# Kernel optimization log

Measured on AMD Instinct MI355X. Metric: run time of the kernel, lower is better.

The kernel has to match this reference:

```python
import jax, jax.numpy as jnp
import numpy as np

NUM_EMBEDDINGS = 8192
EMBEDDING_DIM = 64
COMMITMENT_COST = 0.25


def setup_inputs() -> dict:
    key = jax.random.key(0)
    k1, k2 = jax.random.split(key)
    hidden_states = jax.random.normal(k1, (32, 32, 32, EMBEDDING_DIM), dtype=jnp.float32)
    init_bound = 1.0 / NUM_EMBEDDINGS
    embedding = jax.random.uniform(k2, (NUM_EMBEDDINGS, EMBEDDING_DIM), dtype=jnp.float32,
                                   minval=-init_bound, maxval=init_bound)
    return {"hidden_states": hidden_states, "embedding": embedding}


def reference(hidden_states, embedding):
    # hidden_states: (B, H, W, D); embedding: (K, D)
    flat = hidden_states.reshape(-1, EMBEDDING_DIM)            # (N, D)
    z_sq = jnp.sum(flat * flat, axis=1, keepdims=True)          # (N, 1)
    e_sq = jnp.sum(embedding * embedding, axis=1)               # (K,)
    # squared L2 distances: ||z||^2 + ||e||^2 - 2 z.e
    distances = z_sq + e_sq - 2.0 * (flat @ embedding.T)        # (N, K)
    encoding_indices = jnp.argmin(distances, axis=1)            # (N,)
    # one-hot @ embedding == gather; identical math, efficient form
    quantized = jnp.take(embedding, encoding_indices, axis=0).reshape(hidden_states.shape)
    # codebook + commitment loss (return_loss=True path)
    loss = (jnp.mean((jax.lax.stop_gradient(quantized) - hidden_states) ** 2)
            + COMMITMENT_COST * jnp.mean((quantized - jax.lax.stop_gradient(hidden_states)) ** 2))
    # straight-through estimator
    z_q = hidden_states + jax.lax.stop_gradient(quantized - hidden_states)
    B = hidden_states.shape[0]
    min_encoding_indices = encoding_indices.reshape(B, -1)      # (B, num_tokens)
    return z_q, min_encoding_indices, loss
```

## Files before the change

kernel.cpp:

```cpp
#include <hip/hip_runtime.h>
#include <cfloat>

#define N_TOK   32768
#define DIM     64
#define K_CODES 8192
#define NCHK    64
#define TPB     128

#define IDX_OFF  (N_TOK * DIM)
#define LOSS_OFF (N_TOK * DIM + N_TOK)

#define WS_ESQ   0
#define WS_EHIT  8192
#define WS_PART  270336

#define MRG   2e-5f
#define DINIT 6e-5f

typedef __attribute__((ext_vector_type(8)))  short bf16x8;
typedef __attribute__((ext_vector_type(16))) float f32x16;

__device__ inline ushort f2bf(float x) {
    unsigned u = __float_as_uint(x);
    return (ushort)((u + 0x7FFFu + ((u >> 16) & 1u)) >> 16);
}
__device__ inline float bf2f(ushort h) { return __uint_as_float(((unsigned)h) << 16); }
__device__ inline ushort f2bf_up(float x) {
    unsigned u = __float_as_uint(x);
    return (x >= 0.0f) ? (ushort)((u + 0xFFFFu) >> 16) : (ushort)(u >> 16);
}
__device__ inline unsigned long long packdi(float d, int i) {
    unsigned u = __float_as_uint(d);
    u ^= (u & 0x80000000u) ? 0xFFFFFFFFu : 0x80000000u;
    return ((unsigned long long)u << 32) | (unsigned)i;
}

__global__ __launch_bounds__(256) void esq_kernel(const float* __restrict__ emb,
                                                  float* __restrict__ esq) {
#pragma clang fp contract(off)
    const int tid = threadIdx.x;
    const int q = tid & 7;
    const int code = blockIdx.x * 32 + (tid >> 3);
    const float* row = emb + code * DIM;
    float x = row[q];
    float r = x * x;
#pragma unroll
    for (int m = 1; m < 8; ++m) {
        float y = row[q + 8 * m];
        float sq = y * y;
        r = r + sq;
    }
    r = r + __shfl_xor(r, 1, 64);
    r = r + __shfl_xor(r, 2, 64);
    r = r + __shfl_xor(r, 4, 64);
    if (q == 0) esq[code] = r;
}

__global__ __launch_bounds__(256) void pack2(const float* __restrict__ emb,
                                             ushort* __restrict__ ehiT,
                                             float* __restrict__ eT) {
#pragma clang fp contract(off)
    const int k = blockIdx.x * 256 + threadIdx.x;
    float v[64];
    {
        const float4* ep = (const float4*)(emb + (size_t)k * DIM);
#pragma unroll
        for (int i = 0; i < 16; ++i) {
            const float4 a = ep[i];
            v[4 * i] = a.x; v[4 * i + 1] = a.y; v[4 * i + 2] = a.z; v[4 * i + 3] = a.w;
        }
    }
#pragma unroll
    for (int j = 0; j < 64; ++j) eT[(size_t)j * K_CODES + k] = v[j];
    const int sc = k >> 7, lc = k & 127;
#pragma unroll
    for (int q = 0; q < 4; ++q)
#pragma unroll
        for (int h = 0; h < 2; ++h) {
            bf16x8 o;
#pragma unroll
            for (int e = 0; e < 8; ++e) o[e] = (short)f2bf(v[16 * q + 8 * h + e]);
            *(bf16x8*)(ehiT + ((((size_t)sc * 4 + q) * 2 + h) * 128 + lc) * 8) = o;
        }
}

__global__ __launch_bounds__(256, 2) void vq_mfma(const float* __restrict__ hid,
                                                  const ushort* __restrict__ ehiT,
                                                  ushort* __restrict__ Mm) {
#pragma clang fp contract(off)
    const int tid = threadIdx.x;
    const int lane = tid & 63;
    const int w = tid >> 6;
    const int h = lane >> 5;
    const int t0 = blockIdx.x * 64;

    bf16x8 z_hi[2][4], z_lo[2][4];
#pragma unroll
    for (int ts = 0; ts < 2; ++ts)
#pragma unroll
    for (int q = 0; q < 4; ++q) {
        const float* zp = hid + (size_t)(t0 + 32 * ts + (lane & 31)) * DIM + 16 * q + 8 * h;
        const float4 u0 = *(const float4*)zp;
        const float4 u1 = *(const float4*)(zp + 4);
        const float zz[8] = {u0.x, u0.y, u0.z, u0.w, u1.x, u1.y, u1.z, u1.w};
        bf16x8 hv, lv;
#pragma unroll
        for (int i = 0; i < 8; ++i) {
            const ushort hb = f2bf(zz[i]);
            hv[i] = (short)hb;
            lv[i] = (short)f2bf(zz[i] - bf2f(hb));
        }
        z_hi[ts][q] = hv; z_lo[ts][q] = lv;
    }

    f32x16 zc;
#pragma unroll
    for (int i = 0; i < 16; ++i) zc[i] = 0.0f;

    for (int g = 0; g < 16; ++g) {
        const int sc = 4 * g + w;
        float wm0 = -3.0e38f, wm1 = -3.0e38f;
#pragma unroll
        for (int r = 0; r < 4; ++r) {
            bf16x8 A[4];
#pragma unroll
            for (int q = 0; q < 4; ++q)
                A[q] = *(const bf16x8*)(ehiT +
                        ((((size_t)sc * 4 + q) * 2 + h) * 128 + 32 * r + (lane & 31)) * 8);
            f32x16 d0, d1;
#pragma unroll
            for (int q = 0; q < 4; ++q) {
                if (q == 0) {
                    d0 = __builtin_amdgcn_mfma_f32_32x32x16_bf16(A[0], z_hi[0][0], zc, 0, 0, 0);
                    d1 = __builtin_amdgcn_mfma_f32_32x32x16_bf16(A[0], z_hi[1][0], zc, 0, 0, 0);
                } else {
                    d0 = __builtin_amdgcn_mfma_f32_32x32x16_bf16(A[q], z_hi[0][q], d0, 0, 0, 0);
                    d1 = __builtin_amdgcn_mfma_f32_32x32x16_bf16(A[q], z_hi[1][q], d1, 0, 0, 0);
                }
                d0 = __builtin_amdgcn_mfma_f32_32x32x16_bf16(A[q], z_lo[0][q], d0, 0, 0, 0);
                d1 = __builtin_amdgcn_mfma_f32_32x32x16_bf16(A[q], z_lo[1][q], d1, 0, 0, 0);
            }
#pragma unroll
            for (int i = 0; i < 16; ++i) {
                wm0 = fmaxf(wm0, d0[i]);
                wm1 = fmaxf(wm1, d1[i]);
            }
        }
        wm0 = fmaxf(wm0, __shfl_xor(wm0, 32, 64));
        wm1 = fmaxf(wm1, __shfl_xor(wm1, 32, 64));
        if (lane < 32) {
            Mm[(size_t)sc * N_TOK + t0 + lane]      = f2bf_up(wm0);
            Mm[(size_t)sc * N_TOK + t0 + 32 + lane] = f2bf_up(wm1);
        }
    }
}

__global__ __launch_bounds__(512, 1) void vq_select(const float* __restrict__ hid,
                                                    const float* __restrict__ eT,
                                                    const float* __restrict__ esq,
                                                    const ushort* __restrict__ Mm,
                                                    float* __restrict__ out_idx) {
#pragma clang fp contract(off)
    __shared__ float z_s[TPB][68];
    __shared__ float zsq_s[TPB];
    __shared__ float eps_s[TPB];
    __shared__ float bD_s[TPB];
    __shared__ float mxw[4][TPB];
    __shared__ unsigned long long key_s[TPB];
    __shared__ unsigned long long m0_s[NCHK];
    __shared__ unsigned long long m1_s[NCHK];

    const int tid = threadIdx.x;
    const int lane = tid & 63;
    const int w = tid >> 6;
    const int t0 = blockIdx.x * TPB;

    {
        const int t = tid >> 2;
        const int j4 = (tid & 3) * 4;
        const float4* src = (const float4*)(hid + (size_t)(t0 + t) * DIM);
        float4* dst = (float4*)(&z_s[t][0]);
#pragma unroll
        for (int i = 0; i < 4; ++i) dst[j4 + i] = src[j4 + i];
    }
    if (tid < TPB) key_s[tid] = ~0ull;
    __syncthreads();

    {
        const int token = tid & 127;
        const int cg = tid >> 7;
        float pm = bf2f(Mm[(size_t)(16 * cg) * N_TOK + t0 + token]);
#pragma unroll 5
        for (int c = 16 * cg + 1; c < 16 * cg + 16; ++c)
            pm = fmaxf(pm, bf2f(Mm[(size_t)c * N_TOK + t0 + token]));
        mxw[cg][token] = pm;
    }
    if (tid < TPB) {
        const float* zr = &z_s[tid][0];
        float r[8];
#pragma unroll
        for (int q = 0; q < 8; ++q) {
            float x = zr[q]; r[q] = x * x;
#pragma unroll
            for (int m = 1; m < 8; ++m) {
                float y = zr[q + 8 * m];
                float sq = y * y;
                r[q] = r[q] + sq;
            }
        }
        zsq_s[tid] = ((r[0] + r[1]) + (r[2] + r[3])) + ((r[4] + r[5]) + (r[6] + r[7]));
    }
    __syncthreads();
    if (tid < TPB) {
        const float mx = fmaxf(fmaxf(mxw[0][tid], mxw[1][tid]),
                               fmaxf(mxw[2][tid], mxw[3][tid]));
        const float zsq = zsq_s[tid];
        const float eps = sqrtf(zsq) * 2.5e-6f + 2e-7f;
        eps_s[tid] = eps;
        bD_s[tid] = zsq - 2.0f * mx + 2.0f * eps + DINIT;
    }
    __syncthreads();

#pragma unroll
    for (int i = 0; i < 8; ++i) {
        const int c = 8 * w + i;
        const float mA = bf2f(Mm[(size_t)c * N_TOK + t0 + lane]);
        const int sA = (fmaf(-2.0f, mA + eps_s[lane], zsq_s[lane]) - MRG) < bD_s[lane];
        const unsigned long long b0 = __ballot(sA);
        const float mB = bf2f(Mm[(size_t)c * N_TOK + t0 + 64 + lane]);
        const int sB = (fmaf(-2.0f, mB + eps_s[64 + lane], zsq_s[64 + lane]) - MRG) < bD_s[64 + lane];
        const unsigned long long b1 = __ballot(sB);
        if (lane == 0) { m0_s[c] = b0; m1_s[c] = b1; }
    }

    for (int i = 0; i < 8; ++i) {
        const int c = 8 * w + i;
        unsigned long long msk0 = m0_s[c], msk1 = m1_s[c];
        if (!(msk0 | msk1)) continue;
        const int k0 = c * 128 + 2 * lane;
        const float* eb = eT + k0;
        const float2 es2 = *(const float2*)(esq + k0);

        while (msk0 | msk1) {
            int G = 1;
            int tA, tB;
            if (msk0) { tA = __ffsll(msk0) - 1; msk0 &= msk0 - 1; }
            else      { tA = 64 + __ffsll(msk1) - 1; msk1 &= msk1 - 1; }
            tB = tA;
            if (msk0 | msk1) {
                G = 2;
                if (msk0) { tB = __ffsll(msk0) - 1; msk0 &= msk0 - 1; }
                else      { tB = 64 + __ffsll(msk1) - 1; msk1 &= msk1 - 1; }
            }
            const float4* zpA = (const float4*)(&z_s[tA][0]);
            const float4* zpB = (const float4*)(&z_s[tB][0]);

            float2 bA[8], bB[8];
            float aA0, aA1, aB0, aB1;
#define LOADG(B, G2) { _Pragma("unroll") \
    for (int j = 0; j < 8; ++j) \
        B[j] = *(const float2*)(eb + (size_t)(8 * (G2) + j) * K_CODES); }
#define FMAJ(Bj, vA, vB, COMP) \
    aA0 = fmaf(vA.COMP, Bj.x, aA0); aA1 = fmaf(vA.COMP, Bj.y, aA1); \
    aB0 = fmaf(vB.COMP, Bj.x, aB0); aB1 = fmaf(vB.COMP, Bj.y, aB1);
#define FMAG(B, G2) { \
    const float4 vA = zpA[2 * (G2)], vB = zpB[2 * (G2)]; \
    FMAJ(B[0], vA, vB, x) FMAJ(B[1], vA, vB, y) \
    FMAJ(B[2], vA, vB, z) FMAJ(B[3], vA, vB, w) \
    const float4 uA = zpA[2 * (G2) + 1], uB = zpB[2 * (G2) + 1]; \
    FMAJ(B[4], uA, uB, x) FMAJ(B[5], uA, uB, y) \
    FMAJ(B[6], uA, uB, z) FMAJ(B[7], uA, uB, w) }

            LOADG(bA, 0)
            LOADG(bB, 1)
            {
                const float4 vA = zpA[0], vB = zpB[0];
                aA0 = vA.x * bA[0].x; aA1 = vA.x * bA[0].y;
                aB0 = vB.x * bA[0].x; aB1 = vB.x * bA[0].y;
                FMAJ(bA[1], vA, vB, y)
                FMAJ(bA[2], vA, vB, z)
                FMAJ(bA[3], vA, vB, w)
                const float4 uA = zpA[1], uB = zpB[1];
                FMAJ(bA[4], uA, uB, x)
                FMAJ(bA[5], uA, uB, y)
                FMAJ(bA[6], uA, uB, z)
                FMAJ(bA[7], uA, uB, w)
            }
            LOADG(bA, 2) FMAG(bB, 1)
            LOADG(bB, 3) FMAG(bA, 2)
            LOADG(bA, 4) FMAG(bB, 3)
            LOADG(bB, 5) FMAG(bA, 4)
            LOADG(bA, 6) FMAG(bB, 5)
            LOADG(bB, 7) FMAG(bA, 6)
            FMAG(bB, 7)
#undef LOADG
#undef FMAJ
#undef FMAG

#define FINISH(aX0, aX1, tX) { \
    const float zqX = zsq_s[tX]; \
    const float dX0 = fmaf(-2.0f, aX0, zqX + es2.x); \
    const float dX1 = fmaf(-2.0f, aX1, zqX + es2.y); \
    float dl = dX0; int il = k0; \
    if (dX1 < dl) { dl = dX1; il = k0 + 1; } \
    _Pragma("unroll") \
    for (int mm = 1; mm < 64; mm <<= 1) { \
        const float ov = __shfl_xor(dl, mm, 64); \
        const int   oi = __shfl_xor(il, mm, 64); \
        if (ov < dl || (ov == dl && oi < il)) { dl = ov; il = oi; } \
    } \
    if (lane == 0) atomicMin(&key_s[tX], packdi(dl, il)); }

            FINISH(aA0, aA1, tA)
            if (G > 1) FINISH(aB0, aB1, tB)
#undef FINISH
        }
    }
    __syncthreads();

    if (tid < TPB) out_idx[t0 + tid] = (float)(int)(key_s[tid] & 0xFFFFFFFFull);
}

__global__ __launch_bounds__(256) void vq_finish(const float* __restrict__ hid,
                                                 const float* __restrict__ emb,
                                                 const float* __restrict__ out_idx,
                                                 float* __restrict__ out_zq,
                                                 float* __restrict__ partials) {
#pragma clang fp contract(off)
    __shared__ float lred[4];
    const int tid = threadIdx.x;
    const int t = blockIdx.x * 256 + tid;

    const int bi = (int)out_idx[t];

    const float4* q4 = (const float4*)(emb + (size_t)bi * DIM);
    const float4* h4 = (const float4*)(hid + (size_t)t * DIM);
    float4* o4 = (float4*)(out_zq + (size_t)t * DIM);
    float lsum = 0.f;
#pragma unroll
    for (int i = 0; i < 16; ++i) {
        const float4 q = q4[i];
        const float4 h = h4[i];
        float4 zq;
        float dx;
        dx = q.x - h.x; zq.x = h.x + dx; lsum += dx * dx;
        dx = q.y - h.y; zq.y = h.y + dx; lsum += dx * dx;
        dx = q.z - h.z; zq.z = h.z + dx; lsum += dx * dx;
        dx = q.w - h.w; zq.w = h.w + dx; lsum += dx * dx;
        o4[i] = zq;
    }

#pragma unroll
    for (int off = 32; off >= 1; off >>= 1) lsum += __shfl_xor(lsum, off, 64);
    const int wid = tid >> 6;
    if ((tid & 63) == 0) lred[wid] = lsum;
    __syncthreads();
    if (tid == 0) partials[blockIdx.x] = (lred[0] + lred[1]) + (lred[2] + lred[3]);
}

__global__ __launch_bounds__(128) void loss_kernel(const float* __restrict__ partials,
                                                   float* __restrict__ out_loss) {
#pragma clang fp contract(off)
    __shared__ float s[128];
    const int t = threadIdx.x;
    s[t] = partials[t];
    __syncthreads();
    for (int off = 64; off >= 1; off >>= 1) {
        if (t < off) s[t] = s[t] + s[t + off];
        __syncthreads();
    }
    if (t == 0) {
        const float m = s[0] * (1.0f / 2097152.0f);
        out_loss[0] = m + 0.25f * m;
    }
}

extern "C" void kernel_launch(void* const* d_in, const int* in_sizes, int n_in,
                              void* d_out, int out_size, void* d_ws, size_t ws_size,
                              hipStream_t stream) {
    const float* hid = (const float*)d_in[0];
    const float* emb = (const float*)d_in[1];
    float* out = (float*)d_out;
    float* ws  = (float*)d_ws;
    float*  esq   = ws + WS_ESQ;
    ushort* ehiT  = (ushort*)(ws + WS_EHIT);
    float*  parts = ws + WS_PART;
    float*  eT    = out;
    ushort* Mm    = (ushort*)(out + 524288);

    esq_kernel<<<K_CODES / 32, 256, 0, stream>>>(emb, esq);
    pack2<<<K_CODES / 256, 256, 0, stream>>>(emb, ehiT, eT);
    vq_mfma<<<N_TOK / 64, 256, 0, stream>>>(hid, ehiT, Mm);
    vq_select<<<N_TOK / TPB, 512, 0, stream>>>(hid, eT, esq, Mm, out + IDX_OFF);
    vq_finish<<<N_TOK / 256, 256, 0, stream>>>(hid, emb, out + IDX_OFF, out, parts);
    loss_kernel<<<1, 128, 0, stream>>>(parts, out + LOSS_OFF);
}
```

Measured before the change: 151.5 us.

## Drop bf16 low-part MFMA pass and double-buffer codebook loads in prefilter

The MFMA prefilter kernel stops splitting hidden states into bf16 hi and lo parts and uses only the hi part, which halves the MFMA count. The candidate-selection error bound eps is widened to absorb the extra approximation error. Codebook fragments are now register double-buffered so the next group's loads overlap the current group's MFMAs. The costs are higher register pressure and possibly more candidates passing the filter into the exact refinement stage.

Measured after the change: 138.3 us. 8.7% less time.

```diff
diff --git a/kernel.cpp b/kernel.cpp
--- a/kernel.cpp
+++ b/kernel.cpp
@@ -94,7 +94,7 @@
     const int h = lane >> 5;
     const int t0 = blockIdx.x * 64;
 
-    bf16x8 z_hi[2][4], z_lo[2][4];
+    bf16x8 z_hi[2][4];
 #pragma unroll
     for (int ts = 0; ts < 2; ++ts)
 #pragma unroll
@@ -103,56 +103,61 @@
         const float4 u0 = *(const float4*)zp;
         const float4 u1 = *(const float4*)(zp + 4);
         const float zz[8] = {u0.x, u0.y, u0.z, u0.w, u1.x, u1.y, u1.z, u1.w};
-        bf16x8 hv, lv;
-#pragma unroll
-        for (int i = 0; i < 8; ++i) {
-            const ushort hb = f2bf(zz[i]);
-            hv[i] = (short)hb;
-            lv[i] = (short)f2bf(zz[i] - bf2f(hb));
-        }
-        z_hi[ts][q] = hv; z_lo[ts][q] = lv;
+        bf16x8 hv;
+#pragma unroll
+        for (int i = 0; i < 8; ++i) hv[i] = (short)f2bf(zz[i]);
+        z_hi[ts][q] = hv;
     }
 
     f32x16 zc;
 #pragma unroll
     for (int i = 0; i < 16; ++i) zc[i] = 0.0f;
 
-    for (int g = 0; g < 16; ++g) {
-        const int sc = 4 * g + w;
-        float wm0 = -3.0e38f, wm1 = -3.0e38f;
-#pragma unroll
-        for (int r = 0; r < 4; ++r) {
-            bf16x8 A[4];
-#pragma unroll
-            for (int q = 0; q < 4; ++q)
-                A[q] = *(const bf16x8*)(ehiT +
-                        ((((size_t)sc * 4 + q) * 2 + h) * 128 + 32 * r + (lane & 31)) * 8);
-            f32x16 d0, d1;
-#pragma unroll
-            for (int q = 0; q < 4; ++q) {
-                if (q == 0) {
-                    d0 = __builtin_amdgcn_mfma_f32_32x32x16_bf16(A[0], z_hi[0][0], zc, 0, 0, 0);
-                    d1 = __builtin_amdgcn_mfma_f32_32x32x16_bf16(A[0], z_hi[1][0], zc, 0, 0, 0);
-                } else {
-                    d0 = __builtin_amdgcn_mfma_f32_32x32x16_bf16(A[q], z_hi[0][q], d0, 0, 0, 0);
-                    d1 = __builtin_amdgcn_mfma_f32_32x32x16_bf16(A[q], z_hi[1][q], d1, 0, 0, 0);
-                }
-                d0 = __builtin_amdgcn_mfma_f32_32x32x16_bf16(A[q], z_lo[0][q], d0, 0, 0, 0);
-                d1 = __builtin_amdgcn_mfma_f32_32x32x16_bf16(A[q], z_lo[1][q], d1, 0, 0, 0);
-            }
-#pragma unroll
-            for (int i = 0; i < 16; ++i) {
-                wm0 = fmaxf(wm0, d0[i]);
-                wm1 = fmaxf(wm1, d1[i]);
-            }
-        }
-        wm0 = fmaxf(wm0, __shfl_xor(wm0, 32, 64));
-        wm1 = fmaxf(wm1, __shfl_xor(wm1, 32, 64));
-        if (lane < 32) {
-            Mm[(size_t)sc * N_TOK + t0 + lane]      = f2bf_up(wm0);
-            Mm[(size_t)sc * N_TOK + t0 + 32 + lane] = f2bf_up(wm1);
-        }
-    }
+#define ALOAD(SC, R, Q) (*(const bf16x8*)(ehiT + \
+    ((((size_t)(SC) * 4 + (Q)) * 2 + h) * 128 + 32 * (R) + (lane & 31)) * 8))
+
+    bf16x8 Aa[4][4], Ab[4][4];
+#pragma unroll
+    for (int r = 0; r < 4; ++r)
+#pragma unroll
+        for (int q = 0; q < 4; ++q) Aa[r][q] = ALOAD(w, r, q);
+
+#define MFMA_G(CUR, NXT, G) { \
+    const int sc = 4 * (G) + w; \
+    const int scn = ((G) + 1 < 16) ? (4 * ((G) + 1) + w) : sc; \
+    _Pragma("unroll") \
+    for (int r = 0; r < 4; ++r) \
+        _Pragma("unroll") \
+        for (int q = 0; q < 4; ++q) NXT[r][q] = ALOAD(scn, r, q); \
+    float wm0 = -3.0e38f, wm1 = -3.0e38f; \
+    _Pragma("unroll") \
+    for (int r = 0; r < 4; ++r) { \
+        f32x16 d0 = __builtin_amdgcn_mfma_f32_32x32x16_bf16(CUR[r][0], z_hi[0][0], zc, 0, 0, 0); \
+        f32x16 d1 = __builtin_amdgcn_mfma_f32_32x32x16_bf16(CUR[r][0], z_hi[1][0], zc, 0, 0, 0); \
+        _Pragma("unroll") \
+        for (int q = 1; q < 4; ++q) { \
+            d0 = __builtin_amdgcn_mfma_f32_32x32x16_bf16(CUR[r][q], z_hi[0][q], d0, 0, 0, 0); \
+            d1 = __builtin_amdgcn_mfma_f32_32x32x16_bf16(CUR[r][q], z_hi[1][q], d1, 0, 0, 0); \
+        } \
+        _Pragma("unroll") \
+        for (int i = 0; i < 16; ++i) { \
+            wm0 = fmaxf(wm0, d0[i]); \
+            wm1 = fmaxf(wm1, d1[i]); \
+        } \
+    } \
+    wm0 = fmaxf(wm0, __shfl_xor(wm0, 32, 64)); \
+    wm1 = fmaxf(wm1, __shfl_xor(wm1, 32, 64)); \
+    if (lane < 32) { \
+        Mm[(size_t)sc * N_TOK + t0 + lane]      = f2bf_up(wm0); \
+        Mm[(size_t)sc * N_TOK + t0 + 32 + lane] = f2bf_up(wm1); \
+    } }
+
+    for (int gg = 0; gg < 16; gg += 2) {
+        MFMA_G(Aa, Ab, gg)
+        MFMA_G(Ab, Aa, gg + 1)
+    }
+#undef MFMA_G
+#undef ALOAD
 }
 
 __global__ __launch_bounds__(512, 1) void vq_select(const float* __restrict__ hid,
@@ -215,7 +220,7 @@
         const float mx = fmaxf(fmaxf(mxw[0][tid], mxw[1][tid]),
                                fmaxf(mxw[2][tid], mxw[3][tid]));
         const float zsq = zsq_s[tid];
-        const float eps = sqrtf(zsq) * 2.5e-6f + 2e-7f;
+        const float eps = sqrtf(zsq) * 4.2e-6f + 2e-7f;
         eps_s[tid] = eps;
         bD_s[tid] = zsq - 2.0f * mx + 2.0f * eps + DINIT;
     }
```
